# Optimization experiments

Hardware: AMD Instinct MI355X
Metric: run time of the kernel (lower is better)

The kernel has to match this reference:

```python
import jax, jax.numpy as jnp
import numpy as np
import math

DIM = 1024
INNER = 2048  # must equal seq_len for the original masked_select broadcast to be valid
CAPACITY = 0.25


def _layernorm(x, g, b):
    m = jnp.mean(x, axis=-1, keepdims=True)
    v = jnp.mean((x - m) ** 2, axis=-1, keepdims=True)
    return (x - m) / jnp.sqrt(v + 1e-5) * g + b


def _new_gelu(x):
    c = np.sqrt(2.0 / np.pi).astype(np.float32)
    return 0.5 * x * (1.0 + jnp.tanh(c * (x + 0.044715 * x ** 3)))


def setup_inputs() -> dict:
    key = jax.random.key(0)
    ks = jax.random.split(key, 8)
    b, l, d = 8, 2048, DIM
    f32 = jnp.float32
    rn = lambda k, shape, s=0.02: jax.random.normal(k, shape, dtype=f32) * s
    return {
        "x": jax.random.normal(ks[0], (b, l, d), dtype=f32),
        "router_w": rn(ks[1], (1, d)),
        "router_b": jnp.zeros((1,), f32),
        "ln1_g": jnp.ones((d,), f32),
        "ln1_b": jnp.zeros((d,), f32),
        "wq": rn(ks[2], (INNER, d)),
        "wk": rn(ks[3], (INNER, d)),
        "wv": rn(ks[4], (INNER, d)),
        "ln2_g": jnp.ones((d,), f32),
        "ln2_b": jnp.zeros((d,), f32),
        "fc_w": rn(ks[5], (4 * d, d)),
        "fc_b": jnp.zeros((4 * d,), f32),
        "proj_w": rn(ks[6], (d, 4 * d)),
        "proj_b": jnp.zeros((d,), f32),
    }


def reference(x, router_w, router_b, ln1_g, ln1_b, wq, wk, wv, ln2_g, ln2_b, fc_w, fc_b, proj_w, proj_b):
    b, l, d = x.shape
    router_k = math.ceil(l * CAPACITY)  # static

    # router scores and top-k token selection (sorted=True in torch -> lax.top_k is sorted desc)
    rscore = (x @ router_w.T + router_b)[..., 0]              # [b, l]
    _, topk_idx = jax.lax.top_k(rscore, router_k)             # [b, k]

    h1 = _layernorm(x, ln1_g, ln1_b)

    # masked_select gathers in ascending sequence order -> sort the indices
    sel = jnp.sort(topk_idx, axis=1)                          # [b, k]
    sx = jnp.take_along_axis(h1, sel[:, :, None], axis=1)     # [b, k, d]
    # weight rows selected by the same mask (requires INNER == l)
    q = sx * wq[sel]                                          # [b, k, d]
    kk = sx * wk[sel]
    v = sx * wv[sel]

    scale = 1.0 / jnp.sqrt(jnp.float32(INNER))
    att = jax.nn.softmax(jnp.einsum('bkd,bjd->bkj', q, kk) * scale, axis=-1)
    s_out = jnp.einsum('bkj,bjd->bkd', att, v)                # [b, k, d]

    # scatter back, replicating the original's two sequential indexed writes:
    # output[i, topk_idx[i]] = s_out[i]; then output[i, topk_idx[i]] = x[i, ~topk_idx[i]]
    # (~idx as an index means l-1-idx; the second write overwrites the first)
    bidx = jnp.arange(b)[:, None]
    out = jnp.zeros_like(x).at[bidx, topk_idx].set(s_out)
    rev = jnp.take_along_axis(h1, (l - 1 - topk_idx)[:, :, None], axis=1)
    out = out.at[bidx, topk_idx].set(rev)

    x = x + out

    h2 = _layernorm(x, ln2_g, ln2_b)
    m = _new_gelu(h2 @ fc_w.T + fc_b) @ proj_w.T + proj_b     # dropout = identity (eval)
    return x + m
```

## Files before the change

kernel.cpp:

```cpp
#include <hip/hip_runtime.h>


typedef unsigned short U16;
typedef __attribute__((ext_vector_type(8))) short short8;
typedef __attribute__((ext_vector_type(4))) float f32x4;

__device__ __forceinline__ U16 bf_hi(float f) {
  unsigned u = __float_as_uint(f);
  unsigned r = u + 0x7FFFu + ((u >> 16) & 1u);
  return (U16)(r >> 16);
}

__device__ __forceinline__ float gelu_f(float x) {
  float z = 0.7978845608028654f * (x + 0.044715f * x * x * x);
  float az = fabsf(z);
  float e = __expf(2.0f * az);
  float t = 1.0f - 2.0f / (e + 1.0f);
  t = (z < 0.0f) ? -t : t;
  return 0.5f * x * (1.0f + t);
}

__device__ __forceinline__ void gl_lds16(const void* g, void* l) {
  __builtin_amdgcn_global_load_lds((const __attribute__((address_space(1))) void*)g,
                                   (__attribute__((address_space(3))) void*)l, 16, 0, 0);
}

__device__ __forceinline__ float block_sum(float v, float* sbuf, int tid) {
  #pragma unroll
  for (int o = 32; o > 0; o >>= 1) v += __shfl_down(v, o, 64);
  if ((tid & 63) == 0) sbuf[tid >> 6] = v;
  __syncthreads();
  v = sbuf[0] + sbuf[1] + sbuf[2] + sbuf[3];
  __syncthreads();
  return v;
}

__global__ __launch_bounds__(256) void router_kernel(const float* __restrict__ x,
    const float* __restrict__ rw, const float* __restrict__ rb, float* __restrict__ rs) {
  int w = threadIdx.x >> 6, l = threadIdx.x & 63;
  int t = blockIdx.x * 4 + w;
  const float4* xr  = (const float4*)(x + (size_t)t * 1024);
  const float4* rw4 = (const float4*)rw;
  float s = 0.f;
  #pragma unroll
  for (int i = 0; i < 4; i++) {
    float4 a = xr[l + i * 64], b = rw4[l + i * 64];
    s += a.x * b.x + a.y * b.y + a.z * b.z + a.w * b.w;
  }
  #pragma unroll
  for (int o = 32; o > 0; o >>= 1) s += __shfl_down(s, o, 64);
  if (l == 0) rs[t] = s + rb[0];
}

__global__ __launch_bounds__(1024) void topk_kernel(const float* __restrict__ rscore,
                                                    int* __restrict__ flags) {
  __shared__ float s[2048];
  __shared__ int sFG, sFE;
  int b = blockIdx.x, tid = threadIdx.x;
  const float* rs = rscore + b * 2048;
  s[tid] = rs[tid];
  s[tid + 1024] = rs[tid + 1024];
  if (tid == 0) { sFG = 2048; sFE = 2048; }
  __syncthreads();
  for (int k = 2; k <= 2048; k <<= 1) {
    for (int j = k >> 1; j > 0; j >>= 1) {
      #pragma unroll
      for (int h = 0; h < 2; h++) {
        int i = tid + h * 1024;
        int p = i ^ j;
        if (p > i) {
          float a = s[i], c = s[p];
          bool up = ((i & k) == 0);
          if ((a > c) == up) { s[i] = c; s[p] = a; }
        }
      }
      __syncthreads();
    }
  }
  float T = s[1536];
  #pragma unroll
  for (int h = 0; h < 2; h++) {
    int i = tid + h * 1024;
    float v = s[i];
    if (v > T && (i == 0 || s[i - 1] <= T)) sFG = i;
    if (v == T && (i == 0 || s[i - 1] < T)) sFE = i;
  }
  __syncthreads();
  int cGt = 2048 - sFG;
  int cEq = sFG - sFE;
  int need = 512 - cGt;
  if (need == cEq) {
    #pragma unroll
    for (int h = 0; h < 2; h++) {
      int i = tid + h * 1024;
      flags[b * 2048 + i] = (rs[i] >= T) ? 1 : 0;
    }
  } else if (tid == 0) {
    int taken = 0;
    for (int i = 0; i < 2048; i++) {
      float v = rs[i];
      int f = 0;
      if (v > T) f = 1;
      else if (v == T && taken < need) { f = 1; taken++; }
      flags[b * 2048 + i] = f;
    }
  }
}

__global__ __launch_bounds__(256) void build_x2_ln2(const float* __restrict__ x,
    const int* __restrict__ flags,
    const float* __restrict__ g1, const float* __restrict__ b1,
    const float* __restrict__ g2, const float* __restrict__ b2,
    float* __restrict__ out, U16* __restrict__ h2) {
  int t = blockIdx.x, tid = threadIdx.x;
  __shared__ float sbuf[4];
  float4 xv = *(const float4*)(x + (size_t)t * 1024 + tid * 4);
  float4 x2v = xv;
  if (flags[t]) {
    int i = t >> 11, j = t & 2047;
    const float* xs = x + ((size_t)(i << 11) + (2047 - j)) * 1024;
    float4 sv = *(const float4*)(xs + tid * 4);
    float m = block_sum(sv.x + sv.y + sv.z + sv.w, sbuf, tid) * (1.f / 1024.f);
    float dx = sv.x - m, dy = sv.y - m, dz = sv.z - m, dw = sv.w - m;
    float var = block_sum(dx * dx + dy * dy + dz * dz + dw * dw, sbuf, tid) * (1.f / 1024.f);
    float rstd = rsqrtf(var + 1e-5f);
    float4 gv = *(const float4*)(g1 + tid * 4);
    float4 bv = *(const float4*)(b1 + tid * 4);
    x2v.x += dx * rstd * gv.x + bv.x;
    x2v.y += dy * rstd * gv.y + bv.y;
    x2v.z += dz * rstd * gv.z + bv.z;
    x2v.w += dw * rstd * gv.w + bv.w;
  }
  *(float4*)(out + (size_t)t * 1024 + tid * 4) = x2v;
  float m2 = block_sum(x2v.x + x2v.y + x2v.z + x2v.w, sbuf, tid) * (1.f / 1024.f);
  float dx = x2v.x - m2, dy = x2v.y - m2, dz = x2v.z - m2, dw = x2v.w - m2;
  float var2 = block_sum(dx * dx + dy * dy + dz * dz + dw * dw, sbuf, tid) * (1.f / 1024.f);
  float rstd2 = rsqrtf(var2 + 1e-5f);
  float4 gv = *(const float4*)(g2 + tid * 4);
  float4 bv = *(const float4*)(b2 + tid * 4);
  ushort4 hv;
  hv.x = bf_hi(dx * rstd2 * gv.x + bv.x);
  hv.y = bf_hi(dy * rstd2 * gv.y + bv.y);
  hv.z = bf_hi(dz * rstd2 * gv.z + bv.z);
  hv.w = bf_hi(dw * rstd2 * gv.w + bv.w);
  *(ushort4*)(h2 + (size_t)t * 1024 + tid * 4) = hv;
}

__global__ __launch_bounds__(256) void conv_w(const float* __restrict__ a, U16* __restrict__ o) {
  size_t idx = ((size_t)blockIdx.x * 256 + threadIdx.x) * 4;
  float4 v = *(const float4*)(a + idx);
  ushort4 hv;
  hv.x = bf_hi(v.x); hv.y = bf_hi(v.y); hv.z = bf_hi(v.z); hv.w = bf_hi(v.w);
  *(ushort4*)(o + idx) = hv;
}

template <int KC, int NC, int EPI>
__global__ __launch_bounds__(256) void gemm_bf(
    const U16* __restrict__ A, const U16* __restrict__ B,
    const float* __restrict__ bias, U16* __restrict__ oB, float* __restrict__ oF) {
  __shared__ __align__(16) U16 lds[16384];
  U16* LA = lds;
  U16* LB = lds + 8192;

  int tid = threadIdx.x;
  int w = tid >> 6, l = tid & 63;
  constexpr int nbn = NC / 128;
  int nwg = gridDim.x;
  int wg = blockIdx.x;
  wg = (wg & 7) * (nwg >> 3) + (wg >> 3);
  int tm = wg / nbn, tn = wg % nbn;

  size_t aoff[4], boff[4];
  #pragma unroll
  for (int p = 0; p < 4; p++) {
    int c = p * 256 + tid;
    int r = c >> 3;
    int sl = (c & 7) ^ (r & 7);
    aoff[p] = (size_t)(tm * 128 + r) * KC + sl * 8;
    boff[p] = (size_t)(tn * 128 + r) * KC + sl * 8;
  }

  int wm = w >> 1, wn = w & 1;
  int lr = l & 15, kg = l >> 4;
  int offa[4][2], offb[4][2];
  #pragma unroll
  for (int i = 0; i < 4; i++)
    #pragma unroll
    for (int h = 0; h < 2; h++) {
      int ra = wm * 64 + i * 16 + lr;
      offa[i][h] = ra * 64 + (((h * 4 + kg) ^ (ra & 7)) << 3);
      int rb = wn * 64 + i * 16 + lr;
      offb[i][h] = rb * 64 + (((h * 4 + kg) ^ (rb & 7)) << 3);
    }

  f32x4 acc[4][4];
  #pragma unroll
  for (int i = 0; i < 4; i++)
    #pragma unroll
    for (int j = 0; j < 4; j++) acc[i][j] = {0.f, 0.f, 0.f, 0.f};

  #pragma unroll 1
  for (int kt = 0; kt < KC; kt += 64) {
    #pragma unroll
    for (int p = 0; p < 4; p++) {
      gl_lds16(A + aoff[p] + kt, (char*)LA + (p * 256 + w * 64) * 16);
      gl_lds16(B + boff[p] + kt, (char*)LB + (p * 256 + w * 64) * 16);
    }
    __syncthreads();

    short8 fa[4][2], fb[4][2];
    #pragma unroll
    for (int i = 0; i < 4; i++)
      #pragma unroll
      for (int h = 0; h < 2; h++) {
        fa[i][h] = *(const short8*)(LA + offa[i][h]);
        fb[i][h] = *(const short8*)(LB + offb[i][h]);
      }
    #pragma unroll
    for (int i = 0; i < 4; i++)
      #pragma unroll
      for (int j = 0; j < 4; j++) {
        acc[i][j] = __builtin_amdgcn_mfma_f32_16x16x32_bf16(fa[i][0], fb[j][0], acc[i][j], 0, 0, 0);
        acc[i][j] = __builtin_amdgcn_mfma_f32_16x16x32_bf16(fa[i][1], fb[j][1], acc[i][j], 0, 0, 0);
      }
    __syncthreads();
  }

  int gr0 = tm * 128 + wm * 64 + kg * 4;
  int gc0 = tn * 128 + wn * 64 + lr;
  #pragma unroll
  for (int j = 0; j < 4; j++) {
    int gc = gc0 + j * 16;
    float bv = bias[gc];
    #pragma unroll
    for (int i = 0; i < 4; i++) {
      #pragma unroll
      for (int r = 0; r < 4; r++) {
        size_t o = (size_t)(gr0 + i * 16 + r) * NC + gc;
        float v = acc[i][j][r] + bv;
        if (EPI == 0) {
          oB[o] = bf_hi(gelu_f(v));
        } else {
          oF[o] = oF[o] + v;
        }
      }
    }
  }
}

extern "C" void kernel_launch(void* const* d_in, const int* in_sizes, int n_in,
                              void* d_out, int out_size, void* d_ws, size_t ws_size,
                              hipStream_t stream) {
  const float* x   = (const float*)d_in[0];
  const float* rw  = (const float*)d_in[1];
  const float* rb  = (const float*)d_in[2];
  const float* g1  = (const float*)d_in[3];
  const float* b1  = (const float*)d_in[4];
  const float* g2  = (const float*)d_in[8];
  const float* b2  = (const float*)d_in[9];
  const float* fcw = (const float*)d_in[10];
  const float* fcb = (const float*)d_in[11];
  const float* pjw = (const float*)d_in[12];
  const float* pjb = (const float*)d_in[13];
  float* out = (float*)d_out;
  (void)in_sizes; (void)n_in; (void)out_size;

  const size_t M = 16384;
  char* p = (char*)d_ws;
  U16* h2   = (U16*)p;  p += M * 1024 * 2;
  U16* fw   = (U16*)p;  p += (size_t)4096 * 1024 * 2;
  U16* pw   = (U16*)p;  p += (size_t)4096 * 1024 * 2;
  float* rsc = (float*)p; p += (size_t)8 * 2048 * 4;
  int* flags = (int*)p;   p += (size_t)8 * 2048 * 4;
  size_t fixedB = (size_t)(p - (char*)d_ws);
  U16* act = (U16*)p;

  size_t availB = (ws_size > fixedB) ? (ws_size - fixedB) : 0;
  int CH = 16384;
  while (CH > 2048 && (size_t)CH * 4096 * 2 > availB) CH >>= 1;
  if ((size_t)CH * 4096 * 2 > availB) return;

  router_kernel<<<4096, 256, 0, stream>>>(x, rw, rb, rsc);
  topk_kernel<<<8, 1024, 0, stream>>>(rsc, flags);
  build_x2_ln2<<<16384, 256, 0, stream>>>(x, flags, g1, b1, g2, b2, out, h2);
  conv_w<<<4096, 256, 0, stream>>>(fcw, fw);
  conv_w<<<4096, 256, 0, stream>>>(pjw, pw);

  for (int c0 = 0; c0 < (int)M; c0 += CH) {
    gemm_bf<1024, 4096, 0><<<(CH / 128) * 32, 256, 0, stream>>>(
        h2 + (size_t)c0 * 1024, fw, fcb, act, nullptr);
    gemm_bf<4096, 1024, 1><<<(CH / 128) * 8, 256, 0, stream>>>(
        act, pw, pjb, nullptr, out + (size_t)c0 * 1024);
  }
}
```

Baseline: 602.5 us.

## Double-buffer GEMM LDS with K=32 stages, grouped tile order, fused weight conversion

The bf16 GEMM kernel is restructured to use two 16KB LDS buffers, each holding a 32-wide K slice. The next slice is prefetched via global_load_lds while the current one feeds MFMAs, with s_setprio raised during the MFMA block. Block-to-tile mapping now walks groups of 8 N-tiles to improve L2 reuse. The two weight-conversion launches are merged into one. Halving the K step doubles the number of barriers per tile. Async prefetch overlap relies on the barrier and vmcnt behaviour of the direct-to-LDS loads.

```diff
diff --git a/kernel.cpp b/kernel.cpp
--- a/kernel.cpp
+++ b/kernel.cpp
@@ -146,84 +146,108 @@
   *(ushort4*)(h2 + (size_t)t * 1024 + tid * 4) = hv;
 }
 
-__global__ __launch_bounds__(256) void conv_w(const float* __restrict__ a, U16* __restrict__ o) {
-  size_t idx = ((size_t)blockIdx.x * 256 + threadIdx.x) * 4;
+__global__ __launch_bounds__(256) void conv_w2(const float* __restrict__ a0, U16* __restrict__ o0,
+                                               const float* __restrict__ a1, U16* __restrict__ o1) {
+  int b = blockIdx.x;
+  const float* a = (b < 4096) ? a0 : a1;
+  U16* o = (b < 4096) ? o0 : o1;
+  size_t idx = ((size_t)(b & 4095) * 256 + threadIdx.x) * 4;
   float4 v = *(const float4*)(a + idx);
   ushort4 hv;
   hv.x = bf_hi(v.x); hv.y = bf_hi(v.y); hv.z = bf_hi(v.z); hv.w = bf_hi(v.w);
   *(ushort4*)(o + idx) = hv;
 }
 
-template <int KC, int NC, int EPI>
+template <int KC, int NC, int GRP, int EPI>
 __global__ __launch_bounds__(256) void gemm_bf(
     const U16* __restrict__ A, const U16* __restrict__ B,
     const float* __restrict__ bias, U16* __restrict__ oB, float* __restrict__ oF) {
   __shared__ __align__(16) U16 lds[16384];
-  U16* LA = lds;
-  U16* LB = lds + 8192;
 
   int tid = threadIdx.x;
   int w = tid >> 6, l = tid & 63;
   constexpr int nbn = NC / 128;
   int nwg = gridDim.x;
-  int wg = blockIdx.x;
-  wg = (wg & 7) * (nwg >> 3) + (wg >> 3);
-  int tm = wg / nbn, tn = wg % nbn;
-
-  size_t aoff[4], boff[4];
-  #pragma unroll
-  for (int p = 0; p < 4; p++) {
-    int c = p * 256 + tid;
-    int r = c >> 3;
-    int sl = (c & 7) ^ (r & 7);
+  int nbm = nwg / nbn;
+  int c = (blockIdx.x & 7) * (nwg >> 3) + (blockIdx.x >> 3);
+  int tng = c / (nbm * GRP);
+  int rem = c - tng * (nbm * GRP);
+  int tm = rem / GRP;
+  int tn = tng * GRP + (rem - (rem / GRP) * GRP);
+
+  size_t aoff[2], boff[2];
+  #pragma unroll
+  for (int p = 0; p < 2; p++) {
+    int cc = p * 256 + tid;
+    int r = cc >> 2;
+    int sl = (cc & 3) ^ (r & 3);
     aoff[p] = (size_t)(tm * 128 + r) * KC + sl * 8;
     boff[p] = (size_t)(tn * 128 + r) * KC + sl * 8;
   }
+  char* Lb = (char*)lds;
 
   int wm = w >> 1, wn = w & 1;
   int lr = l & 15, kg = l >> 4;
-  int offa[4][2], offb[4][2];
+  int offa[4], offb[4];
+  #pragma unroll
+  for (int i = 0; i < 4; i++) {
+    int ra = wm * 64 + i * 16 + lr;
+    offa[i] = ra * 32 + ((kg ^ (ra & 3)) << 3);
+    int rb = wn * 64 + i * 16 + lr;
+    offb[i] = 4096 + rb * 32 + ((kg ^ (rb & 3)) << 3);
+  }
+
+  f32x4 acc[4][4];
   #pragma unroll
   for (int i = 0; i < 4; i++)
     #pragma unroll
-    for (int h = 0; h < 2; h++) {
-      int ra = wm * 64 + i * 16 + lr;
-      offa[i][h] = ra * 64 + (((h * 4 + kg) ^ (ra & 7)) << 3);
-      int rb = wn * 64 + i * 16 + lr;
-      offb[i][h] = rb * 64 + (((h * 4 + kg) ^ (rb & 7)) << 3);
-    }
-
-  f32x4 acc[4][4];
-  #pragma unroll
-  for (int i = 0; i < 4; i++)
-    #pragma unroll
     for (int j = 0; j < 4; j++) acc[i][j] = {0.f, 0.f, 0.f, 0.f};
 
+  auto STAGE = [&](int buf, int kt) {
+    char* base = Lb + buf * 16384;
+    #pragma unroll
+    for (int p = 0; p < 2; p++) {
+      gl_lds16(A + aoff[p] + kt, base + (p * 256 + w * 64) * 16);
+      gl_lds16(B + boff[p] + kt, base + 8192 + (p * 256 + w * 64) * 16);
+    }
+  };
+
+  STAGE(0, 0);
+  __syncthreads();
+  int cur = 0;
   #pragma unroll 1
-  for (int kt = 0; kt < KC; kt += 64) {
-    #pragma unroll
-    for (int p = 0; p < 4; p++) {
-      gl_lds16(A + aoff[p] + kt, (char*)LA + (p * 256 + w * 64) * 16);
-      gl_lds16(B + boff[p] + kt, (char*)LB + (p * 256 + w * 64) * 16);
-    }
-    __syncthreads();
-
-    short8 fa[4][2], fb[4][2];
+  for (int kt = 0; kt < KC - 32; kt += 32) {
+    STAGE(cur ^ 1, kt + 32);
+    U16* Lc = lds + cur * 8192;
+    short8 fa[4], fb[4];
+    #pragma unroll
+    for (int i = 0; i < 4; i++) {
+      fa[i] = *(const short8*)(Lc + offa[i]);
+      fb[i] = *(const short8*)(Lc + offb[i]);
+    }
+    __builtin_amdgcn_s_setprio(1);
     #pragma unroll
     for (int i = 0; i < 4; i++)
       #pragma unroll
-      for (int h = 0; h < 2; h++) {
-        fa[i][h] = *(const short8*)(LA + offa[i][h]);
-        fb[i][h] = *(const short8*)(LB + offb[i][h]);
-      }
+      for (int j = 0; j < 4; j++)
+        acc[i][j] = __builtin_amdgcn_mfma_f32_16x16x32_bf16(fa[i], fb[j], acc[i][j], 0, 0, 0);
+    __builtin_amdgcn_s_setprio(0);
+    __syncthreads();
+    cur ^= 1;
+  }
+  {
+    U16* Lc = lds + cur * 8192;
+    short8 fa[4], fb[4];
+    #pragma unroll
+    for (int i = 0; i < 4; i++) {
+      fa[i] = *(const short8*)(Lc + offa[i]);
+      fb[i] = *(const short8*)(Lc + offb[i]);
+    }
     #pragma unroll
     for (int i = 0; i < 4; i++)
       #pragma unroll
-      for (int j = 0; j < 4; j++) {
-        acc[i][j] = __builtin_amdgcn_mfma_f32_16x16x32_bf16(fa[i][0], fb[j][0], acc[i][j], 0, 0, 0);
-        acc[i][j] = __builtin_amdgcn_mfma_f32_16x16x32_bf16(fa[i][1], fb[j][1], acc[i][j], 0, 0, 0);
-      }
-    __syncthreads();
+      for (int j = 0; j < 4; j++)
+        acc[i][j] = __builtin_amdgcn_mfma_f32_16x16x32_bf16(fa[i], fb[j], acc[i][j], 0, 0, 0);
   }
 
   int gr0 = tm * 128 + wm * 64 + kg * 4;
@@ -283,13 +307,12 @@
   router_kernel<<<4096, 256, 0, stream>>>(x, rw, rb, rsc);
   topk_kernel<<<8, 1024, 0, stream>>>(rsc, flags);
   build_x2_ln2<<<16384, 256, 0, stream>>>(x, flags, g1, b1, g2, b2, out, h2);
-  conv_w<<<4096, 256, 0, stream>>>(fcw, fw);
-  conv_w<<<4096, 256, 0, stream>>>(pjw, pw);
+  conv_w2<<<8192, 256, 0, stream>>>(fcw, fw, pjw, pw);
 
   for (int c0 = 0; c0 < (int)M; c0 += CH) {
-    gemm_bf<1024, 4096, 0><<<(CH / 128) * 32, 256, 0, stream>>>(
+    gemm_bf<1024, 4096, 8, 0><<<(CH / 128) * 32, 256, 0, stream>>>(
         h2 + (size_t)c0 * 1024, fw, fcb, act, nullptr);
-    gemm_bf<4096, 1024, 1><<<(CH / 128) * 8, 256, 0, stream>>>(
+    gemm_bf<4096, 1024, 8, 1><<<(CH / 128) * 8, 256, 0, stream>>>(
         act, pw, pjb, nullptr, out + (size_t)c0 * 1024);
   }
 }
```

Result: no change. 608.3 us (+1.0%).
